# Kernel optimization log

Measured on AMD Instinct MI355X. Metric: run time of the kernel, lower is better.

The kernel has to match this reference:

```python
import jax, jax.numpy as jnp
import numpy as np


def setup_inputs() -> dict:
    key = jax.random.key(0)
    k1, k2 = jax.random.split(key)
    B, M, N, D = 64, 16, 64, 1024
    src = jax.random.normal(k1, (B, N, D), dtype=jnp.float32)
    tgts = jax.random.normal(k2, (B, M, N, D), dtype=jnp.float32)
    return {"src": src, "tgts": tgts}


def reference(src, tgts):
    # loss = sum_{b,m,n} | dot(src[b,n], tgts[b,m,n]) |, returned as shape [1]
    dots = jnp.einsum("bnd,bmnd->bmn", src, tgts)  # [B, M, N]
    loss = jnp.sum(jnp.abs(dots))
    return loss.reshape(1)
```

## Files before the change

kernel.cpp:

```cpp
#include <hip/hip_runtime.h>


__global__ __launch_bounds__(256) void orth_loss_kernel(
    const float* __restrict__ src,
    const float* __restrict__ tgts,
    float* __restrict__ out,
    int total_waves)
{
    const int wave = threadIdx.x >> 6;
    const int lane = threadIdx.x & 63;

    float local = 0.0f;

    for (int w = blockIdx.x * 4 + wave; w < total_waves; w += gridDim.x * 4) {
        const int n  = w & 63;
        const int t  = w >> 6;
        const int mh = t & 1;
        const int b  = t >> 1;

        const float4* __restrict__ sp =
            reinterpret_cast<const float4*>(src + ((size_t)(b * 64 + n)) * 1024);
        const float4 s0 = sp[lane];
        const float4 s1 = sp[lane + 64];
        const float4 s2 = sp[lane + 128];
        const float4 s3 = sp[lane + 192];

        const size_t tbase = (((size_t)b * 16 + mh * 8) * 64 + n) * (size_t)1024;

#pragma unroll
        for (int mi = 0; mi < 8; ++mi) {
            const float4* __restrict__ tp =
                reinterpret_cast<const float4*>(tgts + tbase + (size_t)mi * 64 * 1024);
            const float4 t0 = tp[lane];
            const float4 t1 = tp[lane + 64];
            const float4 t2 = tp[lane + 128];
            const float4 t3 = tp[lane + 192];

            float dot = 0.0f;
            dot = fmaf(t0.x, s0.x, dot); dot = fmaf(t0.y, s0.y, dot);
            dot = fmaf(t0.z, s0.z, dot); dot = fmaf(t0.w, s0.w, dot);
            dot = fmaf(t1.x, s1.x, dot); dot = fmaf(t1.y, s1.y, dot);
            dot = fmaf(t1.z, s1.z, dot); dot = fmaf(t1.w, s1.w, dot);
            dot = fmaf(t2.x, s2.x, dot); dot = fmaf(t2.y, s2.y, dot);
            dot = fmaf(t2.z, s2.z, dot); dot = fmaf(t2.w, s2.w, dot);
            dot = fmaf(t3.x, s3.x, dot); dot = fmaf(t3.y, s3.y, dot);
            dot = fmaf(t3.z, s3.z, dot); dot = fmaf(t3.w, s3.w, dot);

#pragma unroll
            for (int off = 32; off > 0; off >>= 1)
                dot += __shfl_down(dot, off, 64);

            if (lane == 0) local += fabsf(dot);
        }
    }

    __shared__ float sbuf[4];
    if (lane == 0) sbuf[wave] = local;
    __syncthreads();

    if (threadIdx.x == 0) {
        const float s = sbuf[0] + sbuf[1] + sbuf[2] + sbuf[3];
        atomicAdd(out, s);
    }
}

extern "C" void kernel_launch(void* const* d_in, const int* in_sizes, int n_in,
                              void* d_out, int out_size, void* d_ws, size_t ws_size,
                              hipStream_t stream) {
    const float* src  = (const float*)d_in[0];
    const float* tgts = (const float*)d_in[1];
    float* out = (float*)d_out;

    const int total_rows  = in_sizes[1] / 1024;
    const int total_waves = total_rows / 8;

    hipMemsetAsync(out, 0, sizeof(float), stream);

    const int blocks = 2048;
    orth_loss_kernel<<<blocks, 256, 0, stream>>>(src, tgts, out, total_waves);
}
```

Before: 60.95 us.

## Process all 16 targets per wave with double-buffered register prefetch

Each wave now handles one (b,n) pair across all 16 target rows instead of half of them, so every src row is loaded once instead of twice. Target loads are double-buffered in registers: the next row is fetched while the current dot product and reduction run. The grid shrinks to one wave per (b,n) pair (1024 blocks) and launch bounds request 4 blocks per CU. The work per wave doubles and register pressure rises from the extra buffer, and there are fewer waves available to hide latency.

```diff
diff --git a/kernel.cpp b/kernel.cpp
--- a/kernel.cpp
+++ b/kernel.cpp
@@ -1,7 +1,7 @@
 #include <hip/hip_runtime.h>
 
 
-__global__ __launch_bounds__(256) void orth_loss_kernel(
+__global__ __launch_bounds__(256, 4) void orth_loss_kernel(
     const float* __restrict__ src,
     const float* __restrict__ tgts,
     float* __restrict__ out,
@@ -13,10 +13,8 @@
     float local = 0.0f;
 
     for (int w = blockIdx.x * 4 + wave; w < total_waves; w += gridDim.x * 4) {
-        const int n  = w & 63;
-        const int t  = w >> 6;
-        const int mh = t & 1;
-        const int b  = t >> 1;
+        const int n = w & 63;
+        const int b = w >> 6;
 
         const float4* __restrict__ sp =
             reinterpret_cast<const float4*>(src + ((size_t)(b * 64 + n)) * 1024);
@@ -25,32 +23,63 @@
         const float4 s2 = sp[lane + 128];
         const float4 s3 = sp[lane + 192];
 
-        const size_t tbase = (((size_t)b * 16 + mh * 8) * 64 + n) * (size_t)1024;
+        const float* __restrict__ trow0 = tgts + (((size_t)b * 16) * 64 + n) * 1024;
+
+        const float4* __restrict__ tp0 = reinterpret_cast<const float4*>(trow0);
+        float4 a0 = tp0[lane];
+        float4 a1 = tp0[lane + 64];
+        float4 a2 = tp0[lane + 128];
+        float4 a3 = tp0[lane + 192];
+        float4 b0, b1, b2, b3;
 
 #pragma unroll
-        for (int mi = 0; mi < 8; ++mi) {
-            const float4* __restrict__ tp =
-                reinterpret_cast<const float4*>(tgts + tbase + (size_t)mi * 64 * 1024);
-            const float4 t0 = tp[lane];
-            const float4 t1 = tp[lane + 64];
-            const float4 t2 = tp[lane + 128];
-            const float4 t3 = tp[lane + 192];
-
-            float dot = 0.0f;
-            dot = fmaf(t0.x, s0.x, dot); dot = fmaf(t0.y, s0.y, dot);
-            dot = fmaf(t0.z, s0.z, dot); dot = fmaf(t0.w, s0.w, dot);
-            dot = fmaf(t1.x, s1.x, dot); dot = fmaf(t1.y, s1.y, dot);
-            dot = fmaf(t1.z, s1.z, dot); dot = fmaf(t1.w, s1.w, dot);
-            dot = fmaf(t2.x, s2.x, dot); dot = fmaf(t2.y, s2.y, dot);
-            dot = fmaf(t2.z, s2.z, dot); dot = fmaf(t2.w, s2.w, dot);
-            dot = fmaf(t3.x, s3.x, dot); dot = fmaf(t3.y, s3.y, dot);
-            dot = fmaf(t3.z, s3.z, dot); dot = fmaf(t3.w, s3.w, dot);
-
+        for (int mi = 0; mi < 16; mi += 2) {
+            {
+                const float4* __restrict__ tpb =
+                    reinterpret_cast<const float4*>(trow0 + (size_t)(mi + 1) * 64 * 1024);
+                b0 = tpb[lane];
+                b1 = tpb[lane + 64];
+                b2 = tpb[lane + 128];
+                b3 = tpb[lane + 192];
+            }
+            {
+                float dot = 0.0f;
+                dot = fmaf(a0.x, s0.x, dot); dot = fmaf(a0.y, s0.y, dot);
+                dot = fmaf(a0.z, s0.z, dot); dot = fmaf(a0.w, s0.w, dot);
+                dot = fmaf(a1.x, s1.x, dot); dot = fmaf(a1.y, s1.y, dot);
+                dot = fmaf(a1.z, s1.z, dot); dot = fmaf(a1.w, s1.w, dot);
+                dot = fmaf(a2.x, s2.x, dot); dot = fmaf(a2.y, s2.y, dot);
+                dot = fmaf(a2.z, s2.z, dot); dot = fmaf(a2.w, s2.w, dot);
+                dot = fmaf(a3.x, s3.x, dot); dot = fmaf(a3.y, s3.y, dot);
+                dot = fmaf(a3.z, s3.z, dot); dot = fmaf(a3.w, s3.w, dot);
 #pragma unroll
-            for (int off = 32; off > 0; off >>= 1)
-                dot += __shfl_down(dot, off, 64);
-
-            if (lane == 0) local += fabsf(dot);
+                for (int off = 32; off > 0; off >>= 1)
+                    dot += __shfl_down(dot, off, 64);
+                if (lane == 0) local += fabsf(dot);
+            }
+            if (mi + 2 < 16) {
+                const float4* __restrict__ tpa =
+                    reinterpret_cast<const float4*>(trow0 + (size_t)(mi + 2) * 64 * 1024);
+                a0 = tpa[lane];
+                a1 = tpa[lane + 64];
+                a2 = tpa[lane + 128];
+                a3 = tpa[lane + 192];
+            }
+            {
+                float dot = 0.0f;
+                dot = fmaf(b0.x, s0.x, dot); dot = fmaf(b0.y, s0.y, dot);
+                dot = fmaf(b0.z, s0.z, dot); dot = fmaf(b0.w, s0.w, dot);
+                dot = fmaf(b1.x, s1.x, dot); dot = fmaf(b1.y, s1.y, dot);
+                dot = fmaf(b1.z, s1.z, dot); dot = fmaf(b1.w, s1.w, dot);
+                dot = fmaf(b2.x, s2.x, dot); dot = fmaf(b2.y, s2.y, dot);
+                dot = fmaf(b2.z, s2.z, dot); dot = fmaf(b2.w, s2.w, dot);
+                dot = fmaf(b3.x, s3.x, dot); dot = fmaf(b3.y, s3.y, dot);
+                dot = fmaf(b3.z, s3.z, dot); dot = fmaf(b3.w, s3.w, dot);
+#pragma unroll
+                for (int off = 32; off > 0; off >>= 1)
+                    dot += __shfl_down(dot, off, 64);
+                if (lane == 0) local += fabsf(dot);
+            }
         }
     }
 
@@ -71,11 +100,10 @@
     const float* tgts = (const float*)d_in[1];
     float* out = (float*)d_out;
 
-    const int total_rows  = in_sizes[1] / 1024;
-    const int total_waves = total_rows / 8;
+    const int total_waves = in_sizes[0] / 1024;
 
     hipMemsetAsync(out, 0, sizeof(float), stream);
 
-    const int blocks = 2048;
+    const int blocks = total_waves / 4;
     orth_loss_kernel<<<blocks, 256, 0, stream>>>(src, tgts, out, total_waves);
 }
```

Result: no change. 59.95 us (-1.6%).
